# Optimization experiments

Measured on AMD Instinct MI355X. Metric: run time of the kernel, lower is better.

## Reference

```python
import jax, jax.numpy as jnp
import numpy as np

B, L, D_FEAT = 16, 2048, 512
H, D_HID, UNITS = 8, 512, 512


def setup_inputs() -> dict:
    key = jax.random.key(0)
    ks = jax.random.split(key, 8)
    s_feat = 1.0 / np.sqrt(D_FEAT)
    s_hid = 1.0 / np.sqrt(D_HID)
    s_u = 1.0 / np.sqrt(UNITS)
    return {
        "features": jax.random.normal(ks[0], (B, L, D_FEAT), jnp.float32),
        "hidden": jax.random.normal(ks[1], (B, H, D_HID), jnp.float32),
        # Per-head Dense params stacked along a leading head axis.
        "W1": jax.random.normal(ks[2], (H, D_FEAT, UNITS), jnp.float32) * s_feat,
        "b1": jnp.zeros((H, UNITS), jnp.float32),
        "W2": jax.random.normal(ks[3], (H, D_HID, UNITS), jnp.float32) * s_hid,
        "b2": jnp.zeros((H, UNITS), jnp.float32),
        "V": jax.random.normal(ks[4], (H, UNITS), jnp.float32) * s_u,
        "bV": jnp.zeros((H,), jnp.float32),
    }


def reference(features, hidden, W1, b1, W2, b2, V, bV):
    # features: [B, L, Df]; hidden: [B, H, Dh]
    # Per-head: tanh(W1(features) + W2(hidden_h)) -> V -> softmax over L -> weighted sum.
    f_proj = jnp.einsum("bld,hdu->bhlu", features, W1) + b1[None, :, None, :]   # [B,H,L,U]
    h_proj = jnp.einsum("bhd,hdu->bhu", hidden, W2) + b2[None, :, :]            # [B,H,U]
    act = jnp.tanh(f_proj + h_proj[:, :, None, :])                               # [B,H,L,U]
    score = jnp.einsum("bhlu,hu->bhl", act, V) + bV[None, :, None]               # [B,H,L]
    attn = jax.nn.softmax(score, axis=-1)                                        # softmax over L
    context = jnp.einsum("bhl,bld->bhd", attn, features)                         # [B,H,Df]
    # Original stacks weights (each [B,L,1]) along axis=2 -> [B,L,H,1]
    attention_weights = jnp.transpose(attn, (0, 2, 1))[..., None]                # [B,L,H,1]
    return context, attention_weights
```

## Files before the change

kernel.cpp:

```cpp
#include <hip/hip_runtime.h>
#include <hip/hip_bf16.h>

#define B_ 16
#define L_ 2048
#define DF 512
#define H_ 8
#define DH 512
#define U_ 512

typedef unsigned short u16;
typedef __attribute__((ext_vector_type(8))) short bf16x8;
typedef __attribute__((ext_vector_type(4))) float f32x4;

__device__ __forceinline__ u16 f2bf(float x) {
  __hip_bfloat16 h = __float2bfloat16(x);
  u16 u;
  __builtin_memcpy(&u, &h, 2);
  return u;
}

__device__ __forceinline__ void load_lds16(const void* g, void* l) {
  __builtin_amdgcn_global_load_lds(
      (const __attribute__((address_space(1))) void*)g,
      (__attribute__((address_space(3))) void*)l, 16, 0, 0);
}

__device__ __forceinline__ float fast_tanh2(float x) {
  float e = __expf(2.f * x);
  return 1.f - __fdividef(2.f, e + 1.f);
}

__global__ __launch_bounds__(256) void convert_kernel(
    const float* __restrict__ F, u16* __restrict__ Abf,
    const float* __restrict__ W1, u16* __restrict__ W1T) {
  __shared__ float t[32][33];
  if (blockIdx.x < 16384) {
    size_t i = ((size_t)blockIdx.x * 256 + threadIdx.x) * 4;
    float4 v = *(const float4*)(F + i);
    ushort4 o;
    o.x = f2bf(v.x); o.y = f2bf(v.y); o.z = f2bf(v.z); o.w = f2bf(v.w);
    *(ushort4*)(Abf + i) = o;
  } else {
    int bid = blockIdx.x - 16384;
    int d0 = (bid & 15) * 32, u0 = ((bid >> 4) & 15) * 32, h = bid >> 8;
    const float* src = W1 + (size_t)h * DF * U_;
    u16* dst = W1T + (size_t)h * U_ * DF;
#pragma unroll
    for (int i = 0; i < 4; ++i) {
      int idx = threadIdx.x + i * 256;
      int r = idx >> 5, c = idx & 31;
      t[r][c] = src[(size_t)(d0 + r) * U_ + u0 + c];
    }
    __syncthreads();
#pragma unroll
    for (int i = 0; i < 4; ++i) {
      int idx = threadIdx.x + i * 256;
      int r = idx >> 5, c = idx & 31;
      dst[(size_t)(u0 + r) * DF + d0 + c] = f2bf(t[c][r]);
    }
  }
}

__global__ __launch_bounds__(128) void hproj_part_kernel(
    const float* __restrict__ hidden, const float* __restrict__ W2,
    float* __restrict__ partial) {
  int h = blockIdx.x;
  int u = blockIdx.y * 128 + threadIdx.x;
  int d0 = blockIdx.z * 64;
  __shared__ float hs[B_][64];
  for (int idx = threadIdx.x; idx < B_ * 64; idx += 128) {
    int b = idx >> 6, d = idx & 63;
    hs[b][d] = hidden[(size_t)(b * H_ + h) * DH + d0 + d];
  }
  __syncthreads();
  float acc[B_];
#pragma unroll
  for (int b = 0; b < B_; b++) acc[b] = 0.f;
  const float* w2p = W2 + ((size_t)h * DH + d0) * U_ + u;
  for (int d = 0; d < 64; d++) {
    float w = w2p[(size_t)d * U_];
#pragma unroll
    for (int b = 0; b < B_; b++) acc[b] += hs[b][d] * w;
  }
#pragma unroll
  for (int b = 0; b < B_; b++)
    partial[(((size_t)blockIdx.z * B_ + b) * H_ + h) * U_ + u] = acc[b];
}

__global__ __launch_bounds__(256) void hproj_combine_kernel(
    const float* __restrict__ partial, const float* __restrict__ b1,
    const float* __restrict__ b2, float* __restrict__ c) {
  int i = blockIdx.x * 256 + threadIdx.x;
  int hu = i & (H_ * U_ - 1);
  float s = b1[hu] + b2[hu];
#pragma unroll
  for (int z = 0; z < 8; z++) s += partial[(size_t)z * B_ * H_ * U_ + i];
  c[i] = s;
}

#define BKS 64

__global__ __launch_bounds__(256, 2) void score_kernel(
    const u16* __restrict__ Abf, const u16* __restrict__ W1T,
    const float* __restrict__ C, const float* __restrict__ V,
    const float* __restrict__ bV, float* __restrict__ score) {
  int l0 = blockIdx.x * 128;
  int b = blockIdx.y, h = blockIdx.z;
  int tid = threadIdx.x;
  int lane = tid & 63, wid = tid >> 6;
  int wr = wid >> 1, wc = wid & 1;
  int rl = lane & 15;
  int khalf = (lane >> 4) << 3;

  __shared__ u16 As[2][128 * BKS];
  __shared__ u16 Bs[2][128 * BKS];
  __shared__ float redsm[2][128];

  const u16* Fb = Abf + (size_t)b * L_ * DF;
  const u16* Wh = W1T + (size_t)h * U_ * DF;
  const float* Cb = C + (size_t)(b * H_ + h) * U_;
  const float* Vh = V + (size_t)h * U_;

  float part[16];
#pragma unroll
  for (int p = 0; p < 16; ++p) part[p] = 0.f;

#define STAGE(buf, kbase)                                                  \
  {                                                                        \
    _Pragma("unroll") for (int i_ = 0; i_ < 4; ++i_) {                     \
      int idx_ = i_ * 256 + tid;                                           \
      int row_ = idx_ >> 3;                                                \
      int ke_ = ((idx_ & 7) ^ (row_ & 7)) << 3;                            \
      load_lds16(Fb + (((size_t)(l0 + row_)) << 9) + (kbase) + ke_,        \
                 &As[buf][idx_ * 8]);                                      \
      load_lds16(Wh + (((size_t)(N0 + row_)) << 9) + (kbase) + ke_,        \
                 &Bs[buf][idx_ * 8]);                                      \
    }                                                                      \
  }

  for (int nc = 0; nc < 4; ++nc) {
    int N0 = nc * 128;
    float cu[4], vv[4];
#pragma unroll
    for (int n = 0; n < 4; ++n) {
      int col = N0 + wc * 64 + n * 16 + rl;
      cu[n] = Cb[col];
      vv[n] = Vh[col];
    }
    f32x4 acc[4][4];
#pragma unroll
    for (int m = 0; m < 4; ++m)
#pragma unroll
      for (int n = 0; n < 4; ++n)
#pragma unroll
        for (int j = 0; j < 4; ++j) acc[m][n][j] = cu[n];

    STAGE(0, 0);
    int cur = 0;
    for (int kt = 0; kt < 8; ++kt) {
      if (kt < 7) {
        STAGE(cur ^ 1, (kt + 1) * BKS);
        asm volatile("s_waitcnt vmcnt(8)" ::: "memory");
      } else {
        asm volatile("s_waitcnt vmcnt(0)" ::: "memory");
      }
      __builtin_amdgcn_s_barrier();
#pragma unroll
      for (int s = 0; s < 2; ++s) {
        bf16x8 bfr[4];
#pragma unroll
        for (int n = 0; n < 4; ++n) {
          int rB = wc * 64 + n * 16 + rl;
          bfr[n] = *(const bf16x8*)&Bs[cur][(rB << 6) +
                                            ((s * 32 + khalf) ^ ((rB & 7) << 3))];
        }
#pragma unroll
        for (int m = 0; m < 4; ++m) {
          int rA = wr * 64 + m * 16 + rl;
          bf16x8 af = *(const bf16x8*)&As[cur][(rA << 6) +
                                               ((s * 32 + khalf) ^
                                                ((rA & 7) << 3))];
#pragma unroll
          for (int n = 0; n < 4; ++n)
            acc[m][n] = __builtin_amdgcn_mfma_f32_16x16x32_bf16(
                af, bfr[n], acc[m][n], 0, 0, 0);
        }
      }
      asm volatile("s_waitcnt lgkmcnt(0)" ::: "memory");
      __builtin_amdgcn_s_barrier();
      cur ^= 1;
    }
#pragma unroll
    for (int n = 0; n < 4; ++n)
#pragma unroll
      for (int m = 0; m < 4; ++m)
#pragma unroll
        for (int j = 0; j < 4; ++j)
          part[m * 4 + j] += fast_tanh2(acc[m][n][j]) * vv[n];
  }
#undef STAGE

#pragma unroll
  for (int p = 0; p < 16; ++p) {
    float v = part[p];
    v += __shfl_xor(v, 1, 64);
    v += __shfl_xor(v, 2, 64);
    v += __shfl_xor(v, 4, 64);
    v += __shfl_xor(v, 8, 64);
    part[p] = v;
  }
  __syncthreads();
  if (rl == 0) {
    int rq = lane >> 4;
#pragma unroll
    for (int m = 0; m < 4; ++m)
#pragma unroll
      for (int j = 0; j < 4; ++j)
        redsm[wc][wr * 64 + m * 16 + rq * 4 + j] = part[m * 4 + j];
  }
  __syncthreads();
  if (tid < 128) {
    float s = redsm[0][tid] + redsm[1][tid] + bV[h];
    score[(size_t)(b * H_ + h) * L_ + l0 + tid] = s;
  }
}

__global__ __launch_bounds__(256) void softmax_kernel(
    const float* __restrict__ score, float* __restrict__ attn,
    float* __restrict__ aw_out) {
  int bh = blockIdx.x;
  int b = bh / H_, h = bh % H_;
  const float* s = score + (size_t)bh * L_;
  __shared__ float sv[L_];
  __shared__ float red[256];

  for (int i = threadIdx.x; i < L_ / 4; i += 256)
    ((float4*)sv)[i] = ((const float4*)s)[i];
  __syncthreads();

  float m = -1e30f;
  for (int l = threadIdx.x; l < L_; l += 256) m = fmaxf(m, sv[l]);
  red[threadIdx.x] = m;
  __syncthreads();
  for (int st = 128; st > 0; st >>= 1) {
    if (threadIdx.x < st)
      red[threadIdx.x] = fmaxf(red[threadIdx.x], red[threadIdx.x + st]);
    __syncthreads();
  }
  m = red[0];
  __syncthreads();

  float sum = 0.f;
  for (int l = threadIdx.x; l < L_; l += 256) sum += __expf(sv[l] - m);
  red[threadIdx.x] = sum;
  __syncthreads();
  for (int st = 128; st > 0; st >>= 1) {
    if (threadIdx.x < st) red[threadIdx.x] += red[threadIdx.x + st];
    __syncthreads();
  }
  float inv = 1.f / red[0];

  for (int l = threadIdx.x; l < L_; l += 256) {
    float a = __expf(sv[l] - m) * inv;
    attn[(size_t)bh * L_ + l] = a;
    aw_out[((size_t)b * L_ + l) * H_ + h] = a;
  }
}

__global__ __launch_bounds__(256) void context_part_kernel(
    const float* __restrict__ F, const float* __restrict__ attn,
    float* __restrict__ partial) {
  int b = blockIdx.x;
  int d0 = blockIdx.y * 64;
  int lz = blockIdx.z;
  int td = threadIdx.x & 63;
  int tl = threadIdx.x >> 6;

  __shared__ float as[H_][256];
  for (int idx = threadIdx.x; idx < H_ * 256; idx += 256)
    as[idx >> 8][idx & 255] =
        attn[((size_t)b * H_ + (idx >> 8)) * L_ + lz * 256 + (idx & 255)];
  __syncthreads();

  float acc[H_] = {};
  for (int l = tl; l < 256; l += 4) {
    float f = F[((size_t)b * L_ + lz * 256 + l) * DF + d0 + td];
#pragma unroll
    for (int h = 0; h < H_; h++) acc[h] += as[h][l] * f;
  }

  __shared__ float red[4][H_][64];
#pragma unroll
  for (int h = 0; h < H_; h++) red[tl][h][td] = acc[h];
  __syncthreads();
  if (tl == 0) {
#pragma unroll
    for (int h = 0; h < H_; h++) {
      float v = red[0][h][td] + red[1][h][td] + red[2][h][td] + red[3][h][td];
      partial[(size_t)lz * B_ * H_ * DF + ((size_t)b * H_ + h) * DF + d0 + td] =
          v;
    }
  }
}

__global__ __launch_bounds__(256) void context_combine_kernel(
    const float* __restrict__ partial, float* __restrict__ ctx_out) {
  int i = blockIdx.x * 256 + threadIdx.x;
  float s = 0.f;
#pragma unroll
  for (int z = 0; z < 8; z++) s += partial[(size_t)z * B_ * H_ * DF + i];
  ctx_out[i] = s;
}

extern "C" void kernel_launch(void* const* d_in, const int* in_sizes, int n_in,
                              void* d_out, int out_size, void* d_ws,
                              size_t ws_size, hipStream_t stream) {
  const float* features = (const float*)d_in[0];
  const float* hidden   = (const float*)d_in[1];
  const float* W1       = (const float*)d_in[2];
  const float* b1       = (const float*)d_in[3];
  const float* W2       = (const float*)d_in[4];
  const float* b2       = (const float*)d_in[5];
  const float* V        = (const float*)d_in[6];
  const float* bV       = (const float*)d_in[7];

  float* out = (float*)d_out;
  float* ctx_out = out;
  float* aw_out  = out + B_ * H_ * DF;

  float* c_buf = (float*)d_ws;
  float* score = c_buf + (size_t)B_ * H_ * U_;
  float* attn  = score + (size_t)B_ * H_ * L_;
  float* hpart = score;
  float* cpart = attn + (size_t)B_ * H_ * L_;
  u16* Abf = (u16*)(cpart + (size_t)8 * B_ * H_ * DF);
  u16* W1T = Abf + (size_t)B_ * L_ * DF;

  convert_kernel<<<16384 + 2048, 256, 0, stream>>>(features, Abf, W1, W1T);
  hproj_part_kernel<<<dim3(H_, U_ / 128, 8), 128, 0, stream>>>(hidden, W2,
                                                               hpart);
  hproj_combine_kernel<<<(B_ * H_ * U_) / 256, 256, 0, stream>>>(hpart, b1, b2,
                                                                 c_buf);
  score_kernel<<<dim3(L_ / 128, B_, H_), 256, 0, stream>>>(Abf, W1T, c_buf, V,
                                                           bV, score);
  softmax_kernel<<<B_ * H_, 256, 0, stream>>>(score, attn, aw_out);
  context_part_kernel<<<dim3(B_, DF / 64, 8), 256, 0, stream>>>(features, attn,
                                                                cpart);
  context_combine_kernel<<<(B_ * H_ * DF) / 256, 256, 0, stream>>>(cpart,
                                                                   ctx_out);
}
```

Before: 233.7 us.

## Enlarge score GEMM tile to 256x256 and split U across blocks

The score kernel now computes a 256-row by 256-unit tile with 512 threads instead of looping over four 128-wide unit chunks, which raises operand reuse per LDS load. The MFMA work is split into quadrant phases separated by barriers, with raised wave priority around the matrix instructions. Each of the two unit-halves writes a partial score, and the softmax kernel adds the two halves while loading. The bV bias is dropped because a constant shift does not change the softmax. In exchange, LDS use roughly doubles and register pressure rises from 32 accumulator tiles per wave, which can reduce occupancy.

New measurement: 274.5 us. 17.4% more time.

```diff
diff --git a/kernel.cpp b/kernel.cpp
--- a/kernel.cpp
+++ b/kernel.cpp
@@ -98,110 +98,136 @@
   c[i] = s;
 }
 
-#define BKS 64
-
-__global__ __launch_bounds__(256, 2) void score_kernel(
+#define BKT 64
+
+__global__ __launch_bounds__(512, 2) void score_kernel(
     const u16* __restrict__ Abf, const u16* __restrict__ W1T,
     const float* __restrict__ C, const float* __restrict__ V,
-    const float* __restrict__ bV, float* __restrict__ score) {
-  int l0 = blockIdx.x * 128;
+    float* __restrict__ pscore) {
+  int gx = blockIdx.x;
+  int mt = gx >> 1, ut = gx & 1;
+  int l0 = mt * 256, u0 = ut * 256;
   int b = blockIdx.y, h = blockIdx.z;
   int tid = threadIdx.x;
   int lane = tid & 63, wid = tid >> 6;
-  int wr = wid >> 1, wc = wid & 1;
-  int rl = lane & 15;
-  int khalf = (lane >> 4) << 3;
-
-  __shared__ u16 As[2][128 * BKS];
-  __shared__ u16 Bs[2][128 * BKS];
-  __shared__ float redsm[2][128];
-
-  const u16* Fb = Abf + (size_t)b * L_ * DF;
-  const u16* Wh = W1T + (size_t)h * U_ * DF;
-  const float* Cb = C + (size_t)(b * H_ + h) * U_;
-  const float* Vh = V + (size_t)h * U_;
-
-  float part[16];
-#pragma unroll
-  for (int p = 0; p < 16; ++p) part[p] = 0.f;
-
-#define STAGE(buf, kbase)                                                  \
+  int wr = wid >> 2, wc = wid & 3;
+  int rl = lane & 15, q = lane >> 4;
+
+  __shared__ u16 As[2][256 * BKT];
+  __shared__ u16 Bs[2][256 * BKT];
+  __shared__ float redsm[4][256];
+
+  const u16* Fb = Abf + ((size_t)b * L_ + l0) * DF;
+  const u16* Wh = W1T + ((size_t)h * U_ + u0) * DF;
+
+  f32x4 acc[8][4];
+#pragma unroll
+  for (int m = 0; m < 8; ++m)
+#pragma unroll
+    for (int n = 0; n < 4; ++n)
+#pragma unroll
+      for (int j = 0; j < 4; ++j) acc[m][n][j] = 0.f;
+
+#define STAGE(bufi, kb)                                                    \
   {                                                                        \
     _Pragma("unroll") for (int i_ = 0; i_ < 4; ++i_) {                     \
-      int idx_ = i_ * 256 + tid;                                           \
+      int idx_ = i_ * 512 + tid;                                           \
       int row_ = idx_ >> 3;                                                \
       int ke_ = ((idx_ & 7) ^ (row_ & 7)) << 3;                            \
-      load_lds16(Fb + (((size_t)(l0 + row_)) << 9) + (kbase) + ke_,        \
-                 &As[buf][idx_ * 8]);                                      \
-      load_lds16(Wh + (((size_t)(N0 + row_)) << 9) + (kbase) + ke_,        \
-                 &Bs[buf][idx_ * 8]);                                      \
+      load_lds16(Fb + ((size_t)row_ << 9) + (kb) + ke_,                    \
+                 &As[bufi][idx_ * 8]);                                     \
+      load_lds16(Wh + ((size_t)row_ << 9) + (kb) + ke_,                    \
+                 &Bs[bufi][idx_ * 8]);                                     \
     }                                                                      \
   }
 
-  for (int nc = 0; nc < 4; ++nc) {
-    int N0 = nc * 128;
-    float cu[4], vv[4];
-#pragma unroll
-    for (int n = 0; n < 4; ++n) {
-      int col = N0 + wc * 64 + n * 16 + rl;
-      cu[n] = Cb[col];
-      vv[n] = Vh[col];
+  bf16x8 a[4][2], bA[2][2], bB[2][2];
+
+#define RD_A(mb)                                                           \
+  {                                                                        \
+    _Pragma("unroll") for (int mm = 0; mm < 4; ++mm)                       \
+    _Pragma("unroll") for (int ss = 0; ss < 2; ++ss) {                     \
+      int rA = wr * 128 + ((mb) + mm) * 16 + rl;                           \
+      a[mm][ss] = *(const bf16x8*)&As[c][(rA << 6) +                       \
+                                         (((ss * 4 + q) ^ (rA & 7)) << 3)];\
+    }                                                                      \
+  }
+
+#define RD_B(arr, nb)                                                      \
+  {                                                                        \
+    _Pragma("unroll") for (int nn = 0; nn < 2; ++nn)                       \
+    _Pragma("unroll") for (int ss = 0; ss < 2; ++ss) {                     \
+      int rB = wc * 64 + ((nb) + nn) * 16 + rl;                            \
+      arr[nn][ss] = *(const bf16x8*)&Bs[c][(rB << 6) +                     \
+                                           (((ss * 4 + q) ^ (rB & 7)) << 3)];\
+    }                                                                      \
+  }
+
+#define MMQ(mb, arr, nb)                                                   \
+  {                                                                        \
+    _Pragma("unroll") for (int ss = 0; ss < 2; ++ss)                       \
+    _Pragma("unroll") for (int mm = 0; mm < 4; ++mm)                       \
+    _Pragma("unroll") for (int nn = 0; nn < 2; ++nn)                       \
+      acc[(mb) + mm][(nb) + nn] = __builtin_amdgcn_mfma_f32_16x16x32_bf16( \
+          a[mm][ss], arr[nn][ss], acc[(mb) + mm][(nb) + nn], 0, 0, 0);     \
+  }
+
+  STAGE(0, 0);
+  asm volatile("s_waitcnt vmcnt(0)" ::: "memory");
+  __builtin_amdgcn_s_barrier();
+  __builtin_amdgcn_sched_barrier(0);
+
+  for (int t = 0; t < 8; ++t) {
+    int c = t & 1;
+    if (t < 7) STAGE(c ^ 1, (t + 1) * BKT);
+    RD_A(0);
+    RD_B(bA, 0);
+    __builtin_amdgcn_s_setprio(1);
+    MMQ(0, bA, 0);
+    __builtin_amdgcn_s_setprio(0);
+    __builtin_amdgcn_s_barrier();
+    RD_B(bB, 2);
+    __builtin_amdgcn_s_setprio(1);
+    MMQ(0, bB, 2);
+    __builtin_amdgcn_s_setprio(0);
+    __builtin_amdgcn_s_barrier();
+    RD_A(4);
+    __builtin_amdgcn_s_setprio(1);
+    MMQ(4, bB, 2);
+    __builtin_amdgcn_s_setprio(0);
+    __builtin_amdgcn_s_barrier();
+    __builtin_amdgcn_s_setprio(1);
+    MMQ(4, bA, 0);
+    __builtin_amdgcn_s_setprio(0);
+    asm volatile("s_waitcnt vmcnt(0)" ::: "memory");
+    __builtin_amdgcn_s_barrier();
+    __builtin_amdgcn_sched_barrier(0);
+  }
+#undef STAGE
+#undef RD_A
+#undef RD_B
+#undef MMQ
+
+  float cu[4], vv[4];
+#pragma unroll
+  for (int n = 0; n < 4; ++n) {
+    int col = u0 + wc * 64 + n * 16 + rl;
+    cu[n] = C[(size_t)(b * H_ + h) * U_ + col];
+    vv[n] = V[h * U_ + col];
+  }
+  float part[32];
+#pragma unroll
+  for (int m = 0; m < 8; ++m)
+#pragma unroll
+    for (int j = 0; j < 4; ++j) {
+      float s = 0.f;
+#pragma unroll
+      for (int n = 0; n < 4; ++n)
+        s += fast_tanh2(acc[m][n][j] + cu[n]) * vv[n];
+      part[m * 4 + j] = s;
     }
-    f32x4 acc[4][4];
-#pragma unroll
-    for (int m = 0; m < 4; ++m)
-#pragma unroll
-      for (int n = 0; n < 4; ++n)
-#pragma unroll
-        for (int j = 0; j < 4; ++j) acc[m][n][j] = cu[n];
-
-    STAGE(0, 0);
-    int cur = 0;
-    for (int kt = 0; kt < 8; ++kt) {
-      if (kt < 7) {
-        STAGE(cur ^ 1, (kt + 1) * BKS);
-        asm volatile("s_waitcnt vmcnt(8)" ::: "memory");
-      } else {
-        asm volatile("s_waitcnt vmcnt(0)" ::: "memory");
-      }
-      __builtin_amdgcn_s_barrier();
-#pragma unroll
-      for (int s = 0; s < 2; ++s) {
-        bf16x8 bfr[4];
-#pragma unroll
-        for (int n = 0; n < 4; ++n) {
-          int rB = wc * 64 + n * 16 + rl;
-          bfr[n] = *(const bf16x8*)&Bs[cur][(rB << 6) +
-                                            ((s * 32 + khalf) ^ ((rB & 7) << 3))];
-        }
-#pragma unroll
-        for (int m = 0; m < 4; ++m) {
-          int rA = wr * 64 + m * 16 + rl;
-          bf16x8 af = *(const bf16x8*)&As[cur][(rA << 6) +
-                                               ((s * 32 + khalf) ^
-                                                ((rA & 7) << 3))];
-#pragma unroll
-          for (int n = 0; n < 4; ++n)
-            acc[m][n] = __builtin_amdgcn_mfma_f32_16x16x32_bf16(
-                af, bfr[n], acc[m][n], 0, 0, 0);
-        }
-      }
-      asm volatile("s_waitcnt lgkmcnt(0)" ::: "memory");
-      __builtin_amdgcn_s_barrier();
-      cur ^= 1;
-    }
-#pragma unroll
-    for (int n = 0; n < 4; ++n)
-#pragma unroll
-      for (int m = 0; m < 4; ++m)
-#pragma unroll
-        for (int j = 0; j < 4; ++j)
-          part[m * 4 + j] += fast_tanh2(acc[m][n][j]) * vv[n];
-  }
-#undef STAGE
-
-#pragma unroll
-  for (int p = 0; p < 16; ++p) {
+#pragma unroll
+  for (int p = 0; p < 32; ++p) {
     float v = part[p];
     v += __shfl_xor(v, 1, 64);
     v += __shfl_xor(v, 2, 64);
@@ -209,33 +235,36 @@
     v += __shfl_xor(v, 8, 64);
     part[p] = v;
   }
-  __syncthreads();
   if (rl == 0) {
-    int rq = lane >> 4;
-#pragma unroll
-    for (int m = 0; m < 4; ++m)
+#pragma unroll
+    for (int m = 0; m < 8; ++m)
 #pragma unroll
       for (int j = 0; j < 4; ++j)
-        redsm[wc][wr * 64 + m * 16 + rq * 4 + j] = part[m * 4 + j];
-  }
-  __syncthreads();
-  if (tid < 128) {
-    float s = redsm[0][tid] + redsm[1][tid] + bV[h];
-    score[(size_t)(b * H_ + h) * L_ + l0 + tid] = s;
+        redsm[wc][wr * 128 + m * 16 + q * 4 + j] = part[m * 4 + j];
+  }
+  __syncthreads();
+  if (tid < 256) {
+    float s = redsm[0][tid] + redsm[1][tid] + redsm[2][tid] + redsm[3][tid];
+    pscore[((size_t)ut * B_ * H_ + b * H_ + h) * L_ + l0 + tid] = s;
   }
 }
 
 __global__ __launch_bounds__(256) void softmax_kernel(
-    const float* __restrict__ score, float* __restrict__ attn,
+    const float* __restrict__ pscore, float* __restrict__ attn,
     float* __restrict__ aw_out) {
   int bh = blockIdx.x;
   int b = bh / H_, h = bh % H_;
-  const float* s = score + (size_t)bh * L_;
+  const float* p0 = pscore + (size_t)bh * L_;
+  const float* p1 = pscore + ((size_t)B_ * H_ + bh) * L_;
   __shared__ float sv[L_];
   __shared__ float red[256];
 
-  for (int i = threadIdx.x; i < L_ / 4; i += 256)
-    ((float4*)sv)[i] = ((const float4*)s)[i];
+  for (int i = threadIdx.x; i < L_ / 4; i += 256) {
+    float4 a = ((const float4*)p0)[i];
+    float4 c = ((const float4*)p1)[i];
+    a.x += c.x; a.y += c.y; a.z += c.z; a.w += c.w;
+    ((float4*)sv)[i] = a;
+  }
   __syncthreads();
 
   float m = -1e30f;
@@ -322,17 +351,16 @@
   const float* W2       = (const float*)d_in[4];
   const float* b2       = (const float*)d_in[5];
   const float* V        = (const float*)d_in[6];
-  const float* bV       = (const float*)d_in[7];
 
   float* out = (float*)d_out;
   float* ctx_out = out;
   float* aw_out  = out + B_ * H_ * DF;
 
-  float* c_buf = (float*)d_ws;
-  float* score = c_buf + (size_t)B_ * H_ * U_;
-  float* attn  = score + (size_t)B_ * H_ * L_;
-  float* hpart = score;
-  float* cpart = attn + (size_t)B_ * H_ * L_;
+  float* c_buf  = (float*)d_ws;
+  float* pscore = c_buf + (size_t)B_ * H_ * U_;
+  float* attn   = pscore;
+  float* hpart  = pscore;
+  float* cpart  = pscore + (size_t)2 * B_ * H_ * L_;
   u16* Abf = (u16*)(cpart + (size_t)8 * B_ * H_ * DF);
   u16* W1T = Abf + (size_t)B_ * L_ * DF;
 
@@ -341,9 +369,9 @@
                                                                hpart);
   hproj_combine_kernel<<<(B_ * H_ * U_) / 256, 256, 0, stream>>>(hpart, b1, b2,
                                                                  c_buf);
-  score_kernel<<<dim3(L_ / 128, B_, H_), 256, 0, stream>>>(Abf, W1T, c_buf, V,
-                                                           bV, score);
-  softmax_kernel<<<B_ * H_, 256, 0, stream>>>(score, attn, aw_out);
+  score_kernel<<<dim3(16, B_, H_), 512, 0, stream>>>(Abf, W1T, c_buf, V,
+                                                     pscore);
+  softmax_kernel<<<B_ * H_, 256, 0, stream>>>(pscore, attn, aw_out);
   context_part_kernel<<<dim3(B_, DF / 64, 8), 256, 0, stream>>>(features, attn,
                                                                 cpart);
   context_combine_kernel<<<(B_ * H_ * DF) / 256, 256, 0, stream>>>(cpart,
```

## Fuse hidden projection into prep kernel and widen score kernel to 8 waves

Applied to the files above, without the earlier changes.

Folds the hidden-projection partial GEMM into the conversion kernel as extra blocks, removing one launch. Moves the score kernel from 4 to 8 waves per block, so each wave handles a 64x32 tile instead of 64x64. This cuts accumulator registers and raises occupancy, at the cost of more B-fragment reuse overhead and a 4-way reduction. It also drops the bV add, which is softmax-invariant, and aliases the attn buffer onto score.

Result: slower. 240.5 us (+2.9%).

```diff
diff --git a/kernel.cpp b/kernel.cpp
--- a/kernel.cpp
+++ b/kernel.cpp
@@ -30,17 +30,20 @@
   return 1.f - __fdividef(2.f, e + 1.f);
 }
 
-__global__ __launch_bounds__(256) void convert_kernel(
+__global__ __launch_bounds__(256) void prep_kernel(
     const float* __restrict__ F, u16* __restrict__ Abf,
-    const float* __restrict__ W1, u16* __restrict__ W1T) {
+    const float* __restrict__ W1, u16* __restrict__ W1T,
+    const float* __restrict__ hidden, const float* __restrict__ W2,
+    float* __restrict__ hpart) {
   __shared__ float t[32][33];
+  __shared__ float hs[B_][64];
   if (blockIdx.x < 16384) {
     size_t i = ((size_t)blockIdx.x * 256 + threadIdx.x) * 4;
     float4 v = *(const float4*)(F + i);
     ushort4 o;
     o.x = f2bf(v.x); o.y = f2bf(v.y); o.z = f2bf(v.z); o.w = f2bf(v.w);
     *(ushort4*)(Abf + i) = o;
-  } else {
+  } else if (blockIdx.x < 18432) {
     int bid = blockIdx.x - 16384;
     int d0 = (bid & 15) * 32, u0 = ((bid >> 4) & 15) * 32, h = bid >> 8;
     const float* src = W1 + (size_t)h * DF * U_;
@@ -58,33 +61,29 @@
       int r = idx >> 5, c = idx & 31;
       dst[(size_t)(u0 + r) * DF + d0 + c] = f2bf(t[c][r]);
     }
-  }
-}
-
-__global__ __launch_bounds__(128) void hproj_part_kernel(
-    const float* __restrict__ hidden, const float* __restrict__ W2,
-    float* __restrict__ partial) {
-  int h = blockIdx.x;
-  int u = blockIdx.y * 128 + threadIdx.x;
-  int d0 = blockIdx.z * 64;
-  __shared__ float hs[B_][64];
-  for (int idx = threadIdx.x; idx < B_ * 64; idx += 128) {
-    int b = idx >> 6, d = idx & 63;
-    hs[b][d] = hidden[(size_t)(b * H_ + h) * DH + d0 + d];
-  }
-  __syncthreads();
-  float acc[B_];
-#pragma unroll
-  for (int b = 0; b < B_; b++) acc[b] = 0.f;
-  const float* w2p = W2 + ((size_t)h * DH + d0) * U_ + u;
-  for (int d = 0; d < 64; d++) {
-    float w = w2p[(size_t)d * U_];
-#pragma unroll
-    for (int b = 0; b < B_; b++) acc[b] += hs[b][d] * w;
-  }
-#pragma unroll
-  for (int b = 0; b < B_; b++)
-    partial[(((size_t)blockIdx.z * B_ + b) * H_ + h) * U_ + u] = acc[b];
+  } else {
+    int bid = blockIdx.x - 18432;
+    int h = bid & 7, uy = (bid >> 3) & 1, dz = bid >> 4;
+    int u = uy * 256 + threadIdx.x;
+    int d0 = dz * 64;
+    for (int idx = threadIdx.x; idx < B_ * 64; idx += 256) {
+      int b = idx >> 6, d = idx & 63;
+      hs[b][d] = hidden[(size_t)(b * H_ + h) * DH + d0 + d];
+    }
+    __syncthreads();
+    float acc[B_];
+#pragma unroll
+    for (int b = 0; b < B_; b++) acc[b] = 0.f;
+    const float* w2p = W2 + ((size_t)h * DH + d0) * U_ + u;
+    for (int d = 0; d < 64; d++) {
+      float w = w2p[(size_t)d * U_];
+#pragma unroll
+      for (int b = 0; b < B_; b++) acc[b] += hs[b][d] * w;
+    }
+#pragma unroll
+    for (int b = 0; b < B_; b++)
+      hpart[(((size_t)dz * B_ + b) * H_ + h) * U_ + u] = acc[b];
+  }
 }
 
 __global__ __launch_bounds__(256) void hproj_combine_kernel(
@@ -100,21 +99,22 @@
 
 #define BKS 64
 
-__global__ __launch_bounds__(256, 2) void score_kernel(
+__global__ __launch_bounds__(512, 4) void score_kernel(
     const u16* __restrict__ Abf, const u16* __restrict__ W1T,
     const float* __restrict__ C, const float* __restrict__ V,
-    const float* __restrict__ bV, float* __restrict__ score) {
+    float* __restrict__ score) {
   int l0 = blockIdx.x * 128;
   int b = blockIdx.y, h = blockIdx.z;
   int tid = threadIdx.x;
   int lane = tid & 63, wid = tid >> 6;
-  int wr = wid >> 1, wc = wid & 1;
+  int wr = wid >> 2, wc = wid & 3;
   int rl = lane & 15;
-  int khalf = (lane >> 4) << 3;
+  int q = lane >> 4;
+  int khalf = q << 3;
 
   __shared__ u16 As[2][128 * BKS];
   __shared__ u16 Bs[2][128 * BKS];
-  __shared__ float redsm[2][128];
+  __shared__ float redsm[4][128];
 
   const u16* Fb = Abf + (size_t)b * L_ * DF;
   const u16* Wh = W1T + (size_t)h * U_ * DF;
@@ -127,8 +127,8 @@
 
 #define STAGE(buf, kbase)                                                  \
   {                                                                        \
-    _Pragma("unroll") for (int i_ = 0; i_ < 4; ++i_) {                     \
-      int idx_ = i_ * 256 + tid;                                           \
+    _Pragma("unroll") for (int i_ = 0; i_ < 2; ++i_) {                     \
+      int idx_ = i_ * 512 + tid;                                           \
       int row_ = idx_ >> 3;                                                \
       int ke_ = ((idx_ & 7) ^ (row_ & 7)) << 3;                            \
       load_lds16(Fb + (((size_t)(l0 + row_)) << 9) + (kbase) + ke_,        \
@@ -140,18 +140,18 @@
 
   for (int nc = 0; nc < 4; ++nc) {
     int N0 = nc * 128;
-    float cu[4], vv[4];
-#pragma unroll
-    for (int n = 0; n < 4; ++n) {
-      int col = N0 + wc * 64 + n * 16 + rl;
+    float cu[2], vv[2];
+#pragma unroll
+    for (int n = 0; n < 2; ++n) {
+      int col = N0 + wc * 32 + n * 16 + rl;
       cu[n] = Cb[col];
       vv[n] = Vh[col];
     }
-    f32x4 acc[4][4];
+    f32x4 acc[4][2];
 #pragma unroll
     for (int m = 0; m < 4; ++m)
 #pragma unroll
-      for (int n = 0; n < 4; ++n)
+      for (int n = 0; n < 2; ++n)
 #pragma unroll
         for (int j = 0; j < 4; ++j) acc[m][n][j] = cu[n];
 
@@ -160,19 +160,20 @@
     for (int kt = 0; kt < 8; ++kt) {
       if (kt < 7) {
         STAGE(cur ^ 1, (kt + 1) * BKS);
-        asm volatile("s_waitcnt vmcnt(8)" ::: "memory");
+        asm volatile("s_waitcnt vmcnt(4)" ::: "memory");
       } else {
         asm volatile("s_waitcnt vmcnt(0)" ::: "memory");
       }
       __builtin_amdgcn_s_barrier();
 #pragma unroll
       for (int s = 0; s < 2; ++s) {
-        bf16x8 bfr[4];
-#pragma unroll
-        for (int n = 0; n < 4; ++n) {
-          int rB = wc * 64 + n * 16 + rl;
+        bf16x8 bfr[2];
+#pragma unroll
+        for (int n = 0; n < 2; ++n) {
+          int rB = wc * 32 + n * 16 + rl;
           bfr[n] = *(const bf16x8*)&Bs[cur][(rB << 6) +
-                                            ((s * 32 + khalf) ^ ((rB & 7) << 3))];
+                                            ((s * 32 + khalf) ^
+                                             ((rB & 7) << 3))];
         }
 #pragma unroll
         for (int m = 0; m < 4; ++m) {
@@ -181,7 +182,7 @@
                                                ((s * 32 + khalf) ^
                                                 ((rA & 7) << 3))];
 #pragma unroll
-          for (int n = 0; n < 4; ++n)
+          for (int n = 0; n < 2; ++n)
             acc[m][n] = __builtin_amdgcn_mfma_f32_16x16x32_bf16(
                 af, bfr[n], acc[m][n], 0, 0, 0);
         }
@@ -191,7 +192,7 @@
       cur ^= 1;
     }
 #pragma unroll
-    for (int n = 0; n < 4; ++n)
+    for (int n = 0; n < 2; ++n)
 #pragma unroll
       for (int m = 0; m < 4; ++m)
 #pragma unroll
@@ -211,16 +212,15 @@
   }
   __syncthreads();
   if (rl == 0) {
-    int rq = lane >> 4;
 #pragma unroll
     for (int m = 0; m < 4; ++m)
 #pragma unroll
       for (int j = 0; j < 4; ++j)
-        redsm[wc][wr * 64 + m * 16 + rq * 4 + j] = part[m * 4 + j];
+        redsm[wc][wr * 64 + m * 16 + q * 4 + j] = part[m * 4 + j];
   }
   __syncthreads();
   if (tid < 128) {
-    float s = redsm[0][tid] + redsm[1][tid] + bV[h];
+    float s = redsm[0][tid] + redsm[1][tid] + redsm[2][tid] + redsm[3][tid];
     score[(size_t)(b * H_ + h) * L_ + l0 + tid] = s;
   }
 }
@@ -322,7 +322,6 @@
   const float* W2       = (const float*)d_in[4];
   const float* b2       = (const float*)d_in[5];
   const float* V        = (const float*)d_in[6];
-  const float* bV       = (const float*)d_in[7];
 
   float* out = (float*)d_out;
   float* ctx_out = out;
@@ -330,19 +329,18 @@
 
   float* c_buf = (float*)d_ws;
   float* score = c_buf + (size_t)B_ * H_ * U_;
-  float* attn  = score + (size_t)B_ * H_ * L_;
+  float* attn  = score;
   float* hpart = score;
-  float* cpart = attn + (size_t)B_ * H_ * L_;
+  float* cpart = score + (size_t)B_ * H_ * L_;
   u16* Abf = (u16*)(cpart + (size_t)8 * B_ * H_ * DF);
   u16* W1T = Abf + (size_t)B_ * L_ * DF;
 
-  convert_kernel<<<16384 + 2048, 256, 0, stream>>>(features, Abf, W1, W1T);
-  hproj_part_kernel<<<dim3(H_, U_ / 128, 8), 128, 0, stream>>>(hidden, W2,
-                                                               hpart);
+  prep_kernel<<<16384 + 2048 + 128, 256, 0, stream>>>(features, Abf, W1, W1T,
+                                                      hidden, W2, hpart);
   hproj_combine_kernel<<<(B_ * H_ * U_) / 256, 256, 0, stream>>>(hpart, b1, b2,
                                                                  c_buf);
-  score_kernel<<<dim3(L_ / 128, B_, H_), 256, 0, stream>>>(Abf, W1T, c_buf, V,
-                                                           bV, score);
+  score_kernel<<<dim3(L_ / 128, B_, H_), 512, 0, stream>>>(Abf, W1T, c_buf, V,
+                                                           score);
   softmax_kernel<<<B_ * H_, 256, 0, stream>>>(score, attn, aw_out);
   context_part_kernel<<<dim3(B_, DF / 64, 8), 256, 0, stream>>>(features, attn,
                                                                 cpart);
```
